# Optimization experiments

Measured on AMD Instinct MI355X. Metric: run time of the kernel, lower is better.

Reference implementation:

```python
import jax, jax.numpy as jnp
import numpy as np
from jax import lax

HEADS = 8
HEAD_C = 16  # attention_channels // heads = 128 // 8


def setup_inputs() -> dict:
    key = jax.random.key(0)
    ks = jax.random.split(key, 16)
    N, I, H, W = 8, 128, 36, 36
    R, C, A, O = 128, 128, 128, 128  # recurrent, common, attention, out channels
    s = lambda *sh: 0.05
    inp = {
        'x': jax.random.normal(ks[0], (N, I, H, W), jnp.float32),
        # input 1x1 conv (Accumulate of single Conv, bias init 0)
        'w_in': jax.random.normal(ks[1], (R, I), jnp.float32) * 0.05,
        'b_in': jnp.zeros((R,), jnp.float32),
        # 3x3 conv on cat([x, h]) -> common channels
        'w_conv': jax.random.normal(ks[2], (C, 2 * R, 3, 3), jnp.float32) * 0.05,
        'b_conv': jnp.zeros((C,), jnp.float32),
        # q/k/v 1x1 projections (no bias)
        'wq': jax.random.normal(ks[3], (A, C), jnp.float32) * 0.05,
        'wk': jax.random.normal(ks[4], (A, C), jnp.float32) * 0.05,
        'wv': jax.random.normal(ks[5], (A, C), jnp.float32) * 0.05,
        # gate 1x1 projections on cat([z, a]) (C + A inputs)
        'w_i': jax.random.normal(ks[6], (R, C + A), jnp.float32) * 0.05,
        'b_i': jnp.full((R,), -1.0, jnp.float32),  # init_input
        'w_f': jax.random.normal(ks[7], (R, C + A), jnp.float32) * 0.05,
        'b_f': jnp.full((R,), 1.0, jnp.float32),   # init_forget
        'w_g': jax.random.normal(ks[8], (R, C + A), jnp.float32) * 0.05,
        'b_g': jnp.zeros((R,), jnp.float32),
        'w_o': jax.random.normal(ks[9], (R, C + A), jnp.float32) * 0.05,
        'b_o': jnp.zeros((R,), jnp.float32),
        # output 1x1 conv
        'w_out': jax.random.normal(ks[10], (O, R), jnp.float32) * 0.05,
        'b_out': jnp.zeros((O,), jnp.float32),
    }
    return inp


def _conv1x1(w, x, b=None):
    y = jnp.einsum('oi,nihw->nohw', w, x)
    if b is not None:
        y = y + b[None, :, None, None]
    return y


def reference(x, w_in, b_in, w_conv, b_conv, wq, wk, wv,
              w_i, b_i, w_f, b_f, w_g, b_g, w_o, b_o, w_out, b_out):
    # first timestep: past is empty -> h = c = 0
    xt = jnp.tanh(_conv1x1(w_in, x, b_in))          # [N, R, H, W]
    h0 = jnp.zeros_like(xt)
    c0 = jnp.zeros_like(xt)
    xh = jnp.concatenate([xt, h0], axis=1)          # groups=1 -> plain concat
    z = lax.conv_general_dilated(xh, w_conv, (1, 1), 'SAME') + b_conv[None, :, None, None]
    N, C, H, W = z.shape
    HW = H * W
    q = _conv1x1(wq, z).reshape(N, HEADS, HEAD_C, HW)
    k = _conv1x1(wk, z).reshape(N, HEADS, HEAD_C, HW)
    v = _conv1x1(wv, z).reshape(N, HEADS, HEAD_C, HW)
    # spatial attention over H*W tokens per head
    w_attn = jax.nn.softmax(jnp.einsum('nhcq,nhcd->nhqd', q, k), axis=-1)  # [N,heads,HW,HW]
    a = jnp.einsum('nhcd,nhqd->nhcq', v, w_attn).reshape(N, -1, H, W)      # [N,A,H,W]
    za = jnp.concatenate([z, a], axis=1)
    i = jax.nn.sigmoid(_conv1x1(w_i, za, b_i))
    f = jax.nn.sigmoid(_conv1x1(w_f, za, b_f))
    g = jnp.tanh(_conv1x1(w_g, za, b_g))
    o = jax.nn.sigmoid(_conv1x1(w_o, za, b_o))
    c = f * c0 + i * g
    h = o * jnp.tanh(c)  # dropout p=0 -> identity
    return _conv1x1(w_out, h, b_out)
```

## Files before the change

kernel.cpp:

```cpp
#include <hip/hip_runtime.h>
#include <hip/hip_bf16.h>
#include <math.h>

typedef __hip_bfloat16 bf16;
typedef __attribute__((ext_vector_type(8))) short frag8;
typedef __attribute__((ext_vector_type(4))) float f32x4;
typedef __attribute__((ext_vector_type(16))) float f32x16;
typedef __attribute__((ext_vector_type(2))) unsigned int u32x2;
typedef __attribute__((ext_vector_type(4))) unsigned int u32x4;

#define HW  1296
#define CH  128
#define TT  1327104

__device__ __forceinline__ float b2f(bf16 v) { return __bfloat162float(v); }
__device__ __forceinline__ float bits2f(unsigned short u) {
    return __uint_as_float(((unsigned)u) << 16);
}
__device__ __forceinline__ float frcp(float x) { return __builtin_amdgcn_rcpf(x); }
__device__ __forceinline__ float fsigm(float x) { return frcp(1.0f + __expf(-x)); }
__device__ __forceinline__ float ftanh(float x) {
    float xc = fminf(15.0f, fmaxf(-15.0f, x));
    float e = __expf(2.0f * xc);
    return (e - 1.0f) * frcp(e + 1.0f);
}
__device__ __forceinline__ int packrh(float a, float b) {
    unsigned ua = __float_as_uint(a) + 0x8000u;
    unsigned ub = __float_as_uint(b) + 0x8000u;
    return (int)__builtin_amdgcn_perm(ub, ua, 0x07060302);
}
__device__ __forceinline__ int2 pack4(float a, float b, float c, float d) {
    int2 r; r.x = packrh(a, b); r.y = packrh(c, d); return r;
}
__device__ __forceinline__ unsigned cvtpk(float a, float b) {
    unsigned r;
    asm("v_cvt_pk_bf16_f32 %0, %1, %2" : "=v"(r) : "v"(a), "v"(b));
    return r;
}

__device__ __forceinline__ int detect_f32(const void* w) {
    const short4* p = (const short4*)w;
    short4 v = p[threadIdx.x & 63];
    int bad = 0;
    #pragma unroll
    for (int j = 0; j < 4; ++j) {
        float f = bits2f(((const unsigned short*)&v)[j]);
        if (!(fabsf(f) <= 100.0f)) bad = 1;
    }
    return __any(bad) ? 1 : 0;
}

__global__ __launch_bounds__(256) void k_prep(
    const void* w_in, const void* w_conv, const void* wq, const void* wk, const void* wv,
    const void* w_i, const void* w_g, const void* w_o, const void* w_out,
    const void* b_in, const void* b_conv, const void* b_i, const void* b_g,
    const void* b_o, const void* b_out,
    bf16* __restrict__ Wdst, float* __restrict__ Bdst)
{
    int idx = blockIdx.x * 256 + threadIdx.x;
    const int f = detect_f32(w_in);
    if (idx < 327680) {
        const void* src; int si;
        if (idx < 16384)       { src = w_in; si = idx; }
        else if (idx < 163840) { int j = idx - 16384; int tap = j >> 14, rem = j & 16383;
                                 int o = rem >> 7, r = rem & 127;
                                 src = w_conv; si = o * 2304 + r * 9 + tap; }
        else if (idx < 212992) { int j = idx - 163840; int o = j >> 7, i = j & 127;
                                 int ws_ = o >> 7;
                                 src = ws_ == 0 ? wq : ws_ == 1 ? wk : wv;
                                 si = (o & 127) * 128 + i; }
        else if (idx < 311296) { int j = idx - 212992; int g = j >> 15, rem = j & 32767;
                                 int o = rem >> 8, k = rem & 255;
                                 src = g == 0 ? w_i : g == 1 ? w_g : w_o; si = o * 256 + k; }
        else                   { int j = idx - 311296; int o = j >> 7, i = j & 127;
                                 src = w_out; si = o * 128 + i; }
        float v = f ? ((const float*)src)[si] : b2f(((const bf16*)src)[si]);
        if (idx >= 163840 && idx < 180224) v *= 1.4426950408889634f;
        Wdst[idx] = __float2bfloat16(v);
    } else if (idx < 327680 + 768) {
        int j = idx - 327680; int b = j >> 7, e = j & 127;
        const void* src = b == 0 ? b_in : b == 1 ? b_conv : b == 2 ? b_i
                        : b == 3 ? b_g : b == 4 ? b_o : b_out;
        Bdst[j] = f ? ((const float*)src)[e] : b2f(((const bf16*)src)[e]);
    }
}

__global__ __launch_bounds__(256) void k_inm(const void* __restrict__ x,
                                             const void* __restrict__ wraw,
                                             const bf16* __restrict__ Wm,
                                             const float* __restrict__ bias,
                                             bf16* __restrict__ XT) {
    __shared__ short Xl[32][132];
    const int tid = threadIdx.x, wave = tid >> 6, lane = tid & 63;
    const int quad = lane >> 4, l16 = lane & 15;
    const int n = blockIdx.x;
    const int pbase = blockIdx.y * 32;
    const int obase = blockIdx.z * 32 + (wave & 1) * 16;
    const int pstrip = (wave >> 1) * 16;
    const int f = detect_f32(wraw);

    frag8 WF[4];
    #pragma unroll
    for (int kc = 0; kc < 4; ++kc)
        WF[kc] = *(const frag8*)&Wm[(obase + l16) * CH + kc * 32 + quad * 8];

    #pragma unroll
    for (int rep = 0; rep < 4; ++rep) {
        int u = tid + rep * 256;
        int i = u >> 3;
        int p4 = (u & 7) * 4;
        int p = pbase + p4;
        short4 s = {0, 0, 0, 0};
        if (p < HW) {
            size_t gi = (size_t)n * CH * HW + (size_t)i * HW + p;
            if (f) {
                float4 fv = *(const float4*)((const float*)x + gi);
                int2 pk = pack4(fv.x, fv.y, fv.z, fv.w);
                s = *(short4*)&pk;
            } else {
                s = *(const short4*)((const bf16*)x + gi);
            }
        }
        Xl[p4 + 0][i] = s.x; Xl[p4 + 1][i] = s.y;
        Xl[p4 + 2][i] = s.z; Xl[p4 + 3][i] = s.w;
    }
    __syncthreads();

    const int pl = pstrip + l16;
    f32x4 acc = {0.f, 0.f, 0.f, 0.f};
    #pragma unroll
    for (int kc = 0; kc < 4; ++kc) {
        int k = kc * 32 + quad * 8;
        short4 b0 = *(const short4*)&Xl[pl][k];
        short4 b1 = *(const short4*)&Xl[pl][k + 4];
        frag8 bf = {b0.x, b0.y, b0.z, b0.w, b1.x, b1.y, b1.z, b1.w};
        acc = __builtin_amdgcn_mfma_f32_16x16x32_bf16(WF[kc], bf, acc, 0, 0, 0);
    }

    int p = pbase + pstrip + l16;
    if (p < HW) {
        int og = obase + quad * 4;
        int2 pk = pack4(ftanh(acc[0] + bias[og + 0]), ftanh(acc[1] + bias[og + 1]),
                        ftanh(acc[2] + bias[og + 2]), ftanh(acc[3] + bias[og + 3]));
        *(int2*)((short*)XT + ((size_t)n * HW + p) * CH + og) = pk;
    }
}

__global__ __launch_bounds__(256) void k_conv(
    const bf16* __restrict__ Act, const bf16* __restrict__ Wm,
    const float* __restrict__ bias, bf16* __restrict__ o0)
{
    const int tid = threadIdx.x, wave = tid >> 6, lane = tid & 63;
    const int quad = lane >> 4, l16 = lane & 15;
    const int ostrip = wave & 1, pstrip = wave >> 1;
    const int n = blockIdx.x;
    const int obase = blockIdx.z * 32 + ostrip * 16;
    const int pbase = blockIdx.y * 64 + pstrip * 32;
    const bf16* actn = Act + (size_t)n * HW * CH;

    const int p1 = pbase + l16, p2 = pbase + 16 + l16;
    const bool p1ok = p1 < HW, p2ok = p2 < HW;
    const int h1 = p1 / 36, w1 = p1 - h1 * 36;
    const int h2 = p2 / 36, w2 = p2 - h2 * 36;

    frag8 zf = {0, 0, 0, 0, 0, 0, 0, 0};
    f32x4 acc[2];
    acc[0] = (f32x4){0.f, 0.f, 0.f, 0.f};
    acc[1] = (f32x4){0.f, 0.f, 0.f, 0.f};

    frag8 A1[2][4], A2[2][4], WT[2][4];

    #define LOADTAP(TAP, BUF)                                                        \
    {                                                                                \
        const int dy = (TAP) / 3 - 1, dx = (TAP) - ((TAP) / 3) * 3 - 1;              \
        const bool ok1 = p1ok && (unsigned)(h1 + dy) < 36u && (unsigned)(w1 + dx) < 36u; \
        const bool ok2 = p2ok && (unsigned)(h2 + dy) < 36u && (unsigned)(w2 + dx) < 36u; \
        const int sh = dy * 36 + dx;                                                 \
        const bf16* a1 = actn + (size_t)(p1 + sh) * CH + quad * 8;                   \
        const bf16* a2 = actn + (size_t)(p2 + sh) * CH + quad * 8;                   \
        const bf16* wp = Wm + (TAP) * 16384 + (obase + l16) * CH + quad * 8;         \
        _Pragma("unroll")                                                            \
        for (int kc = 0; kc < 4; ++kc) {                                             \
            A1[BUF][kc] = ok1 ? *(const frag8*)&a1[kc * 32] : zf;                    \
            A2[BUF][kc] = ok2 ? *(const frag8*)&a2[kc * 32] : zf;                    \
            WT[BUF][kc] = *(const frag8*)&wp[kc * 32];                               \
        }                                                                            \
    }

    LOADTAP(0, 0);
    #pragma unroll
    for (int tap = 0; tap < 9; ++tap) {
        const int cur = tap & 1;
        if (tap < 8) LOADTAP(tap + 1, cur ^ 1);
        #pragma unroll
        for (int kc = 0; kc < 4; ++kc) {
            acc[0] = __builtin_amdgcn_mfma_f32_16x16x32_bf16(WT[cur][kc], A1[cur][kc], acc[0], 0, 0, 0);
            acc[1] = __builtin_amdgcn_mfma_f32_16x16x32_bf16(WT[cur][kc], A2[cur][kc], acc[1], 0, 0, 0);
        }
    }
    #undef LOADTAP

    const int og = obase + quad * 4;
    #pragma unroll
    for (int pt = 0; pt < 2; ++pt) {
        int p = pbase + pt * 16 + l16;
        if (p >= HW) continue;
        size_t rowoff = ((size_t)n * HW + p) * CH;
        int2 pk = pack4(acc[pt][0] + bias[og + 0], acc[pt][1] + bias[og + 1],
                        acc[pt][2] + bias[og + 2], acc[pt][3] + bias[og + 3]);
        *(int2*)((short*)o0 + rowoff + og) = pk;
    }
}

__global__ __launch_bounds__(256) void k_qkv(
    const bf16* __restrict__ Act, const bf16* __restrict__ Wm,
    bf16* __restrict__ o0, bf16* __restrict__ o1, bf16* __restrict__ o2)
{
    const int tid = threadIdx.x, wave = tid >> 6, lane = tid & 63;
    const int quad = lane >> 4, l16 = lane & 15;
    const int ostrip = wave & 1, pstrip = wave >> 1;
    const int n = blockIdx.x;
    const int obase = blockIdx.z * 64 + ostrip * 32;
    const int pbase = blockIdx.y * 64 + pstrip * 32;
    const bf16* actn = Act + (size_t)n * HW * CH;
    const bool vtile = (blockIdx.z >= 4);

    const int p1 = pbase + l16, p2 = pbase + 16 + l16;
    const bool p1ok = p1 < HW, p2ok = p2 < HW;

    frag8 zf = {0, 0, 0, 0, 0, 0, 0, 0};
    frag8 B1[4], B2[4], W0a[4], W1a[4];
    #pragma unroll
    for (int kc = 0; kc < 4; ++kc) {
        int ko = kc * 32 + quad * 8;
        B1[kc] = p1ok ? *(const frag8*)&actn[(size_t)p1 * CH + ko] : zf;
        B2[kc] = p2ok ? *(const frag8*)&actn[(size_t)p2 * CH + ko] : zf;
        W0a[kc] = *(const frag8*)&Wm[(size_t)(obase + l16) * CH + ko];
        W1a[kc] = *(const frag8*)&Wm[(size_t)(obase + 16 + l16) * CH + ko];
    }

    f32x4 acc[2][2];
    #pragma unroll
    for (int of = 0; of < 2; ++of) {
        acc[of][0] = (f32x4){0.f, 0.f, 0.f, 0.f};
        acc[of][1] = (f32x4){0.f, 0.f, 0.f, 0.f};
    }

    #pragma unroll
    for (int kc = 0; kc < 4; ++kc) {
        if (vtile) {
            acc[0][0] = __builtin_amdgcn_mfma_f32_16x16x32_bf16(B1[kc], W0a[kc], acc[0][0], 0, 0, 0);
            acc[0][1] = __builtin_amdgcn_mfma_f32_16x16x32_bf16(B2[kc], W0a[kc], acc[0][1], 0, 0, 0);
            acc[1][0] = __builtin_amdgcn_mfma_f32_16x16x32_bf16(B1[kc], W1a[kc], acc[1][0], 0, 0, 0);
            acc[1][1] = __builtin_amdgcn_mfma_f32_16x16x32_bf16(B2[kc], W1a[kc], acc[1][1], 0, 0, 0);
        } else {
            acc[0][0] = __builtin_amdgcn_mfma_f32_16x16x32_bf16(W0a[kc], B1[kc], acc[0][0], 0, 0, 0);
            acc[0][1] = __builtin_amdgcn_mfma_f32_16x16x32_bf16(W0a[kc], B2[kc], acc[0][1], 0, 0, 0);
            acc[1][0] = __builtin_amdgcn_mfma_f32_16x16x32_bf16(W1a[kc], B1[kc], acc[1][0], 0, 0, 0);
            acc[1][1] = __builtin_amdgcn_mfma_f32_16x16x32_bf16(W1a[kc], B2[kc], acc[1][1], 0, 0, 0);
        }
    }

    if (vtile) {
        #pragma unroll
        for (int of = 0; of < 2; ++of) {
            int ov = obase + of * 16 - 256 + l16;
            #pragma unroll
            for (int pt = 0; pt < 2; ++pt) {
                int p4 = pbase + pt * 16 + quad * 4;
                if (p4 >= HW) continue;
                int2 pk = pack4(acc[of][pt][0], acc[of][pt][1], acc[of][pt][2], acc[of][pt][3]);
                *(int2*)((short*)o2 + ((size_t)n * CH + ov) * HW + p4) = pk;
            }
        }
        return;
    }
    #pragma unroll
    for (int of = 0; of < 2; ++of) {
        int og = obase + of * 16 + quad * 4;
        int which = og >> 7, ol = og & 127;
        bf16* dst = which == 0 ? o0 : o1;
        #pragma unroll
        for (int pt = 0; pt < 2; ++pt) {
            int p = pbase + pt * 16 + l16;
            if (p >= HW) continue;
            size_t di = (((size_t)n * 8 + (ol >> 4)) * HW + p) * 16 + (ol & 15);
            int2 pk = pack4(acc[of][pt][0], acc[of][pt][1], acc[of][pt][2], acc[of][pt][3]);
            *(int2*)((short*)dst + di) = pk;
        }
    }
}

__global__ __launch_bounds__(256) void k_cell(
    const bf16* __restrict__ Zb, const bf16* __restrict__ Ab,
    const bf16* __restrict__ Wg, const float* __restrict__ bg,
    const bf16* __restrict__ Wo, const float* __restrict__ bo,
    void* __restrict__ out, const void* __restrict__ wraw)
{
    __shared__ short Hl[16][136];
    const int tid = threadIdx.x, w = tid >> 6, lane = tid & 63;
    const int quad = lane >> 4, l16 = lane & 15;
    const int n = blockIdx.x;
    const int pbase = blockIdx.y * 16;
    const int f32f = detect_f32(wraw);
    const bf16* zn = Zb + (size_t)n * HW * CH;
    const bf16* an = Ab + (size_t)n * HW * CH;

    const int obase = w * 32;
    const int p1 = pbase + l16;

    f32x4 acc[3][2];
    #pragma unroll
    for (int g = 0; g < 3; ++g) {
        acc[g][0] = (f32x4){0.f, 0.f, 0.f, 0.f};
        acc[g][1] = (f32x4){0.f, 0.f, 0.f, 0.f};
    }

    frag8 GB[2];
    frag8 GW[2][6];

    #define LOADG(KC, BUF)                                                           \
    {                                                                                \
        const bf16* src = ((KC) >= 4) ? an : zn;                                     \
        const int ko = ((KC) & 3) * 32 + quad * 8;                                   \
        GB[BUF] = *(const frag8*)&src[(size_t)p1 * CH + ko];                         \
        _Pragma("unroll")                                                            \
        for (int g = 0; g < 3; ++g) {                                                \
            _Pragma("unroll")                                                        \
            for (int of = 0; of < 2; ++of)                                           \
                GW[BUF][g * 2 + of] = *(const frag8*)&Wg[g * 32768 +                 \
                    (obase + of * 16 + l16) * 256 + (KC) * 32 + quad * 8];           \
        }                                                                            \
    }

    LOADG(0, 0);
    #pragma unroll
    for (int kc = 0; kc < 8; ++kc) {
        const int cur = kc & 1;
        if (kc < 7) LOADG(kc + 1, cur ^ 1);
// ... 22 lines not shown
        *(int2*)&Hl[l16][og] = pack4(hv[0], hv[1], hv[2], hv[3]);
    }

    frag8 OW[2][4];
    #pragma unroll
    for (int of = 0; of < 2; ++of)
        #pragma unroll
        for (int kc = 0; kc < 4; ++kc)
            OW[of][kc] = *(const frag8*)&Wo[(size_t)(obase + of * 16 + l16) * CH
                                            + kc * 32 + quad * 8];
    __syncthreads();

    f32x4 oc[2];
    oc[0] = (f32x4){0.f, 0.f, 0.f, 0.f};
    oc[1] = (f32x4){0.f, 0.f, 0.f, 0.f};
    #pragma unroll
    for (int kc = 0; kc < 4; ++kc) {
        int k = kc * 32 + quad * 8;
        short4 h0 = *(const short4*)&Hl[l16][k];
        short4 h1 = *(const short4*)&Hl[l16][k + 4];
        frag8 af = {h0.x, h0.y, h0.z, h0.w, h1.x, h1.y, h1.z, h1.w};
        #pragma unroll
        for (int of = 0; of < 2; ++of)
            oc[of] = __builtin_amdgcn_mfma_f32_16x16x32_bf16(af, OW[of][kc], oc[of], 0, 0, 0);
    }
    int p4 = pbase + quad * 4;
    #pragma unroll
    for (int of = 0; of < 2; ++of) {
        int o = obase + of * 16 + l16;
        float bv = bo[o];
        size_t di = ((size_t)n * CH + o) * HW + p4;
        if (f32f) {
            float4 fv = {oc[of][0] + bv, oc[of][1] + bv, oc[of][2] + bv, oc[of][3] + bv};
            *(float4*)&((float*)out)[di] = fv;
        } else {
            int2 pk = pack4(oc[of][0] + bv, oc[of][1] + bv, oc[of][2] + bv, oc[of][3] + bv);
            *(int2*)&((short*)out)[di] = pk;
        }
    }
}

__global__ __launch_bounds__(512) void k_attn(const bf16* __restrict__ Qg,
                                              const bf16* __restrict__ Kg,
                                              const bf16* __restrict__ Vcf,
                                              bf16* __restrict__ A) {
    __shared__ float Lc[4][9][64];

    const int tid = threadIdx.x;
    const int w = tid >> 6, lane = tid & 63;
    const int l32 = lane & 31, hi = lane >> 5;
    const int qw = w & 3, dq = w >> 2;
    const int n = blockIdx.x;
    const int head = blockIdx.z;
    const int qb = blockIdx.y * 128 + qw * 32;
    const int qtok = qb + l32;

    const short* Qh = (const short*)Qg + ((size_t)(n * 8 + head)) * HW * 16;
    const short* Kh = (const short*)Kg + ((size_t)(n * 8 + head)) * HW * 16;
    const short* Vh = (const short*)Vcf + ((size_t)n * CH + head * 16) * HW;

    frag8 qf = {0, 0, 0, 0, 0, 0, 0, 0};
    if (qtok < HW) qf = *(const frag8*)&Qh[(size_t)qtok * 16 + hi * 8];

    const short one = (short)0x3F80;
    const frag8 vones = {one, one, one, one, one, one, one, one};
    const frag8 vzero = {0, 0, 0, 0, 0, 0, 0, 0};
    const frag8 vfill = (l32 == 16) ? vones : vzero;
    const bool vload = l32 < 16;
    const short* Vrow = Vh + (size_t)(vload ? l32 : 0) * HW;

    const f32x16 zero16 = {};
    f32x16 Oacc = {};

    auto KLD = [&](int dd) -> frag8 {
        return *(const frag8*)&Kh[(size_t)(dd + l32) * 16 + hi * 8];
    };
    auto VLD = [&](int dd) -> frag8 {
        return vload ? *(const frag8*)&Vrow[dd + hi * 8] : vfill;
    };

    const int c0 = dq ? 20 : 0;
    frag8 kf  = KLD(c0 * 32);
    frag8 kf2 = KLD(c0 * 32 + 32);
    frag8 va  = VLD(c0 * 32);
    frag8 vb  = VLD(c0 * 32 + 16);
    f32x16 S = __builtin_amdgcn_mfma_f32_32x32x16_bf16(kf, qf, zero16, 0, 0, 0);

    for (int it = 0; it < 20; ++it) {
        const int d0 = (c0 + it) * 32;
        frag8 kn  = KLD(d0 + 64);
        frag8 van = VLD(d0 + 32);
        frag8 vbn = VLD(d0 + 48);
        f32x16 Sn = __builtin_amdgcn_mfma_f32_32x32x16_bf16(kf2, qf, zero16, 0, 0, 0);

        float p[16];
        #pragma unroll
        for (int r = 0; r < 16; ++r) p[r] = __builtin_amdgcn_exp2f(S[r]);

        #pragma unroll
        for (int hh = 0; hh < 2; ++hh) {
            unsigned P0 = cvtpk(p[hh * 8 + 0], p[hh * 8 + 1]);
            unsigned P1 = cvtpk(p[hh * 8 + 2], p[hh * 8 + 3]);
            unsigned P2 = cvtpk(p[hh * 8 + 4], p[hh * 8 + 5]);
            unsigned P3 = cvtpk(p[hh * 8 + 6], p[hh * 8 + 7]);
            u32x2 s02 = __builtin_amdgcn_permlane32_swap(P0, P2, false, false);
            u32x2 s13 = __builtin_amdgcn_permlane32_swap(P1, P3, false, false);
            u32x4 bw = {s02[0], s13[0], s02[1], s13[1]};
            frag8 pf = __builtin_bit_cast(frag8, bw);
            Oacc = __builtin_amdgcn_mfma_f32_32x32x16_bf16(hh ? vb : va, pf, Oacc, 0, 0, 0);
        }
        kf2 = kn; va = van; vb = vbn; S = Sn;
    }

    if (dq) {
        float p[8];
        #pragma unroll
        for (int r = 0; r < 8; ++r) p[r] = __builtin_amdgcn_exp2f(S[r]);
        unsigned P0 = cvtpk(p[0], p[1]);
        unsigned P1 = cvtpk(p[2], p[3]);
        unsigned P2 = cvtpk(p[4], p[5]);
        unsigned P3 = cvtpk(p[6], p[7]);
        u32x2 s02 = __builtin_amdgcn_permlane32_swap(P0, P2, false, false);
        u32x2 s13 = __builtin_amdgcn_permlane32_swap(P1, P3, false, false);
        u32x4 bw = {s02[0], s13[0], s02[1], s13[1]};
        frag8 pf = __builtin_bit_cast(frag8, bw);
        Oacc = __builtin_amdgcn_mfma_f32_32x32x16_bf16(va, pf, Oacc, 0, 0, 0);
        #pragma unroll
        for (int r = 0; r < 8; ++r) Lc[qw][r][lane] = Oacc[r];
        Lc[qw][8][lane] = Oacc[8];
    }
    __syncthreads();
    if (dq == 0) {
        #pragma unroll
        for (int r = 0; r < 8; ++r) Oacc[r] += Lc[qw][r][lane];
        float lsum = Oacc[8] + Lc[qw][8][lane];
        u32x2 lb = __builtin_amdgcn_permlane32_swap(__float_as_uint(lsum),
                                                    __float_as_uint(lsum), false, false);
        float inv = frcp(__uint_as_float(lb[0]));
        if (qtok < HW) {
            short* An = (short*)A + ((size_t)n * HW + qtok) * CH + head * 16;
            int2 pk0 = pack4(Oacc[0] * inv, Oacc[1] * inv, Oacc[2] * inv, Oacc[3] * inv);
            int2 pk1 = pack4(Oacc[4] * inv, Oacc[5] * inv, Oacc[6] * inv, Oacc[7] * inv);
            *(int2*)&An[hi * 4] = pk0;
            *(int2*)&An[8 + hi * 4] = pk1;
        }
    }
}

extern "C" void kernel_launch(void* const* d_in, const int* in_sizes, int n_in,
                              void* d_out, int out_size, void* d_ws, size_t ws_size,
                              hipStream_t stream) {
    char* ws = (char*)d_ws;
    bf16*  Wst  = (bf16*)(ws + 256);
    float* Bst  = (float*)(ws + 655616);
    bf16*  XT   = (bf16*)(ws + 1048576);
    bf16*  Zb   = XT + TT;
    bf16*  Qb   = Zb + TT;
    bf16*  Kb   = Qb + TT;
    bf16*  Vb   = Kb + TT;
    bf16*  Ab   = Vb + TT;

    k_prep<<<1284, 256, 0, stream>>>(d_in[1], d_in[3], d_in[5], d_in[6], d_in[7],
                                     d_in[8], d_in[12], d_in[14], d_in[16],
                                     d_in[2], d_in[4], d_in[9], d_in[13], d_in[15], d_in[17],
                                     Wst, Bst);
    k_inm<<<dim3(8, 41, 4), 256, 0, stream>>>(d_in[0], d_in[1], Wst, Bst, XT);
    k_conv<<<dim3(8, 21, 4), 256, 0, stream>>>(XT, Wst + 16384, Bst + 128, Zb);
    k_qkv<<<dim3(8, 21, 6), 256, 0, stream>>>(Zb, Wst + 163840, Qb, Kb, Vb);
    k_attn<<<dim3(8, 11, 8), 512, 0, stream>>>(Qb, Kb, Vb, Ab);
    k_cell<<<dim3(8, 81), 256, 0, stream>>>(Zb, Ab, Wst + 212992, Bst + 256,
                                            Wst + 311296, Bst + 640, d_out, d_in[1]);
}
```

Before: 195.2 us.

## Fuse all stages into one persistent cooperative kernel with grid syncs

Replaces six separate kernel launches with a single cooperative persistent kernel (768 blocks of 256 threads) that loops over each stage's tiles and separates stages with grid-wide barriers. The attention stage is also reshaped from 512-thread blocks covering 128 queries to 256-thread blocks covering 64 queries. The aim is to remove launch gaps and inter-kernel drain between the short stages. In exchange, grid syncs add cost, the fixed grid may give uneven load balance per stage, and register pressure from merging all stages could lower occupancy; a non-cooperative multi-launch path is kept as a fallback.

```diff
diff --git a/kernel.cpp b/kernel.cpp
--- a/kernel.cpp
+++ b/kernel.cpp
@@ -1,4 +1,5 @@
 #include <hip/hip_runtime.h>
+#include <hip/hip_cooperative_groups.h>
 #include <hip/hip_bf16.h>
 #include <math.h>
 
@@ -50,54 +51,51 @@
     return __any(bad) ? 1 : 0;
 }
 
-__global__ __launch_bounds__(256) void k_prep(
-    const void* w_in, const void* w_conv, const void* wq, const void* wk, const void* wv,
-    const void* w_i, const void* w_g, const void* w_o, const void* w_out,
-    const void* b_in, const void* b_conv, const void* b_i, const void* b_g,
-    const void* b_o, const void* b_out,
-    bf16* __restrict__ Wdst, float* __restrict__ Bdst)
-{
-    int idx = blockIdx.x * 256 + threadIdx.x;
-    const int f = detect_f32(w_in);
+struct MP {
+    const void *x, *w_in, *w_conv, *wq, *wk, *wv, *w_i, *w_g, *w_o, *w_out;
+    const void *b_in, *b_conv, *b_i, *b_g, *b_o, *b_out;
+    bf16* Wst; float* Bst;
+    bf16 *XT, *Zb, *Qb, *Kb, *Vb, *Ab;
+    void* out;
+};
+
+__device__ __forceinline__ void dev_prep(const MP& p, int idx, int f) {
     if (idx < 327680) {
         const void* src; int si;
-        if (idx < 16384)       { src = w_in; si = idx; }
+        if (idx < 16384)       { src = p.w_in; si = idx; }
         else if (idx < 163840) { int j = idx - 16384; int tap = j >> 14, rem = j & 16383;
                                  int o = rem >> 7, r = rem & 127;
-                                 src = w_conv; si = o * 2304 + r * 9 + tap; }
+                                 src = p.w_conv; si = o * 2304 + r * 9 + tap; }
         else if (idx < 212992) { int j = idx - 163840; int o = j >> 7, i = j & 127;
                                  int ws_ = o >> 7;
-                                 src = ws_ == 0 ? wq : ws_ == 1 ? wk : wv;
+                                 src = ws_ == 0 ? p.wq : ws_ == 1 ? p.wk : p.wv;
                                  si = (o & 127) * 128 + i; }
         else if (idx < 311296) { int j = idx - 212992; int g = j >> 15, rem = j & 32767;
                                  int o = rem >> 8, k = rem & 255;
-                                 src = g == 0 ? w_i : g == 1 ? w_g : w_o; si = o * 256 + k; }
+                                 src = g == 0 ? p.w_i : g == 1 ? p.w_g : p.w_o;
+                                 si = o * 256 + k; }
         else                   { int j = idx - 311296; int o = j >> 7, i = j & 127;
-                                 src = w_out; si = o * 128 + i; }
+                                 src = p.w_out; si = o * 128 + i; }
         float v = f ? ((const float*)src)[si] : b2f(((const bf16*)src)[si]);
         if (idx >= 163840 && idx < 180224) v *= 1.4426950408889634f;
-        Wdst[idx] = __float2bfloat16(v);
+        p.Wst[idx] = __float2bfloat16(v);
     } else if (idx < 327680 + 768) {
         int j = idx - 327680; int b = j >> 7, e = j & 127;
-        const void* src = b == 0 ? b_in : b == 1 ? b_conv : b == 2 ? b_i
-                        : b == 3 ? b_g : b == 4 ? b_o : b_out;
-        Bdst[j] = f ? ((const float*)src)[e] : b2f(((const bf16*)src)[e]);
-    }
-}
-
-__global__ __launch_bounds__(256) void k_inm(const void* __restrict__ x,
-                                             const void* __restrict__ wraw,
-                                             const bf16* __restrict__ Wm,
-                                             const float* __restrict__ bias,
-                                             bf16* __restrict__ XT) {
-    __shared__ short Xl[32][132];
+        const void* src = b == 0 ? p.b_in : b == 1 ? p.b_conv : b == 2 ? p.b_i
+                        : b == 3 ? p.b_g : b == 4 ? p.b_o : p.b_out;
+        p.Bst[j] = f ? ((const float*)src)[e] : b2f(((const bf16*)src)[e]);
+    }
+}
+
+__device__ __forceinline__ void dev_inm(const MP& p, int f, int n, int py, int oz,
+                                        short (*Xl)[132]) {
     const int tid = threadIdx.x, wave = tid >> 6, lane = tid & 63;
     const int quad = lane >> 4, l16 = lane & 15;
-    const int n = blockIdx.x;
-    const int pbase = blockIdx.y * 32;
-    const int obase = blockIdx.z * 32 + (wave & 1) * 16;
+    const int pbase = py * 32;
+    const int obase = oz * 32 + (wave & 1) * 16;
     const int pstrip = (wave >> 1) * 16;
-    const int f = detect_f32(wraw);
+    const bf16* Wm = p.Wst;
+    const float* bias = p.Bst;
 
     frag8 WF[4];
     #pragma unroll
@@ -109,16 +107,16 @@
         int u = tid + rep * 256;
         int i = u >> 3;
         int p4 = (u & 7) * 4;
-        int p = pbase + p4;
+        int pp = pbase + p4;
         short4 s = {0, 0, 0, 0};
-        if (p < HW) {
-            size_t gi = (size_t)n * CH * HW + (size_t)i * HW + p;
+        if (pp < HW) {
+            size_t gi = (size_t)n * CH * HW + (size_t)i * HW + pp;
             if (f) {
-                float4 fv = *(const float4*)((const float*)x + gi);
+                float4 fv = *(const float4*)((const float*)p.x + gi);
                 int2 pk = pack4(fv.x, fv.y, fv.z, fv.w);
                 s = *(short4*)&pk;
             } else {
-                s = *(const short4*)((const bf16*)x + gi);
+                s = *(const short4*)((const bf16*)p.x + gi);
             }
         }
         Xl[p4 + 0][i] = s.x; Xl[p4 + 1][i] = s.y;
@@ -137,26 +135,25 @@
         acc = __builtin_amdgcn_mfma_f32_16x16x32_bf16(WF[kc], bf, acc, 0, 0, 0);
     }
 
-    int p = pbase + pstrip + l16;
-    if (p < HW) {
+    int pp = pbase + pstrip + l16;
+    if (pp < HW) {
         int og = obase + quad * 4;
         int2 pk = pack4(ftanh(acc[0] + bias[og + 0]), ftanh(acc[1] + bias[og + 1]),
                         ftanh(acc[2] + bias[og + 2]), ftanh(acc[3] + bias[og + 3]));
-        *(int2*)((short*)XT + ((size_t)n * HW + p) * CH + og) = pk;
-    }
-}
-
-__global__ __launch_bounds__(256) void k_conv(
-    const bf16* __restrict__ Act, const bf16* __restrict__ Wm,
-    const float* __restrict__ bias, bf16* __restrict__ o0)
-{
+        *(int2*)((short*)p.XT + ((size_t)n * HW + pp) * CH + og) = pk;
+    }
+    __syncthreads();
+}
+
+__device__ __forceinline__ void dev_conv(const MP& p, int n, int py, int oz) {
     const int tid = threadIdx.x, wave = tid >> 6, lane = tid & 63;
     const int quad = lane >> 4, l16 = lane & 15;
     const int ostrip = wave & 1, pstrip = wave >> 1;
-    const int n = blockIdx.x;
-    const int obase = blockIdx.z * 32 + ostrip * 16;
-    const int pbase = blockIdx.y * 64 + pstrip * 32;
-    const bf16* actn = Act + (size_t)n * HW * CH;
+    const int obase = oz * 32 + ostrip * 16;
+    const int pbase = py * 64 + pstrip * 32;
+    const bf16* Wm = p.Wst + 16384;
+    const float* bias = p.Bst + 128;
+    const bf16* actn = p.XT + (size_t)n * HW * CH;
 
     const int p1 = pbase + l16, p2 = pbase + 16 + l16;
     const bool p1ok = p1 < HW, p2ok = p2 < HW;
@@ -203,27 +200,24 @@
     const int og = obase + quad * 4;
     #pragma unroll
     for (int pt = 0; pt < 2; ++pt) {
-        int p = pbase + pt * 16 + l16;
-        if (p >= HW) continue;
-        size_t rowoff = ((size_t)n * HW + p) * CH;
+        int pp = pbase + pt * 16 + l16;
+        if (pp >= HW) continue;
+        size_t rowoff = ((size_t)n * HW + pp) * CH;
         int2 pk = pack4(acc[pt][0] + bias[og + 0], acc[pt][1] + bias[og + 1],
                         acc[pt][2] + bias[og + 2], acc[pt][3] + bias[og + 3]);
-        *(int2*)((short*)o0 + rowoff + og) = pk;
-    }
-}
-
-__global__ __launch_bounds__(256) void k_qkv(
-    const bf16* __restrict__ Act, const bf16* __restrict__ Wm,
-    bf16* __restrict__ o0, bf16* __restrict__ o1, bf16* __restrict__ o2)
-{
+        *(int2*)((short*)p.Zb + rowoff + og) = pk;
+    }
+}
+
+__device__ __forceinline__ void dev_qkv(const MP& p, int n, int py, int oz) {
     const int tid = threadIdx.x, wave = tid >> 6, lane = tid & 63;
     const int quad = lane >> 4, l16 = lane & 15;
     const int ostrip = wave & 1, pstrip = wave >> 1;
-    const int n = blockIdx.x;
-    const int obase = blockIdx.z * 64 + ostrip * 32;
-    const int pbase = blockIdx.y * 64 + pstrip * 32;
-    const bf16* actn = Act + (size_t)n * HW * CH;
-    const bool vtile = (blockIdx.z >= 4);
+    const int obase = oz * 64 + ostrip * 32;
+    const int pbase = py * 64 + pstrip * 32;
+    const bf16* Wm = p.Wst + 163840;
+    const bf16* actn = p.Zb + (size_t)n * HW * CH;
+    const bool vtile = (oz >= 4);
 
     const int p1 = pbase + l16, p2 = pbase + 16 + l16;
     const bool p1ok = p1 < HW, p2ok = p2 < HW;
@@ -270,7 +264,7 @@
                 int p4 = pbase + pt * 16 + quad * 4;
                 if (p4 >= HW) continue;
                 int2 pk = pack4(acc[of][pt][0], acc[of][pt][1], acc[of][pt][2], acc[of][pt][3]);
-                *(int2*)((short*)o2 + ((size_t)n * CH + ov) * HW + p4) = pk;
+                *(int2*)((short*)p.Vb + ((size_t)n * CH + ov) * HW + p4) = pk;
             }
         }
         return;
@@ -279,32 +273,131 @@
     for (int of = 0; of < 2; ++of) {
         int og = obase + of * 16 + quad * 4;
         int which = og >> 7, ol = og & 127;
-        bf16* dst = which == 0 ? o0 : o1;
+        bf16* dst = which == 0 ? p.Qb : p.Kb;
         #pragma unroll
         for (int pt = 0; pt < 2; ++pt) {
-            int p = pbase + pt * 16 + l16;
-            if (p >= HW) continue;
-            size_t di = (((size_t)n * 8 + (ol >> 4)) * HW + p) * 16 + (ol & 15);
+            int pp = pbase + pt * 16 + l16;
+            if (pp >= HW) continue;
+            size_t di = (((size_t)n * 8 + (ol >> 4)) * HW + pp) * 16 + (ol & 15);
             int2 pk = pack4(acc[of][pt][0], acc[of][pt][1], acc[of][pt][2], acc[of][pt][3]);
             *(int2*)((short*)dst + di) = pk;
         }
     }
 }
 
-__global__ __launch_bounds__(256) void k_cell(
-    const bf16* __restrict__ Zb, const bf16* __restrict__ Ab,
-    const bf16* __restrict__ Wg, const float* __restrict__ bg,
-    const bf16* __restrict__ Wo, const float* __restrict__ bo,
-    void* __restrict__ out, const void* __restrict__ wraw)
-{
-    __shared__ short Hl[16][136];
+__device__ __forceinline__ void dev_attn(const MP& p, int n, int qt, int head,
+                                         float (*Lc)[9][64]) {
+    const int tid = threadIdx.x;
+    const int w = tid >> 6, lane = tid & 63;
+    const int l32 = lane & 31, hi = lane >> 5;
+    const int qw = w & 1, dq = w >> 1;
+    const int qb = qt * 64 + qw * 32;
+    const int qtok = qb + l32;
+
+    const short* Qh = (const short*)p.Qb + ((size_t)(n * 8 + head)) * HW * 16;
+    const short* Kh = (const short*)p.Kb + ((size_t)(n * 8 + head)) * HW * 16;
+    const short* Vh = (const short*)p.Vb + ((size_t)n * CH + head * 16) * HW;
+
+    frag8 qf = {0, 0, 0, 0, 0, 0, 0, 0};
+    if (qtok < HW) qf = *(const frag8*)&Qh[(size_t)qtok * 16 + hi * 8];
+
+    const short one = (short)0x3F80;
+    const frag8 vones = {one, one, one, one, one, one, one, one};
+    const frag8 vzero = {0, 0, 0, 0, 0, 0, 0, 0};
+    const frag8 vfill = (l32 == 16) ? vones : vzero;
+    const bool vload = l32 < 16;
+    const short* Vrow = Vh + (size_t)(vload ? l32 : 0) * HW;
+
+    const f32x16 zero16 = {};
+    f32x16 Oacc = {};
+
+    auto KLD = [&](int dd) -> frag8 {
+        return *(const frag8*)&Kh[(size_t)(dd + l32) * 16 + hi * 8];
+    };
+    auto VLD = [&](int dd) -> frag8 {
+        return vload ? *(const frag8*)&Vrow[dd + hi * 8] : vfill;
+    };
+
+    const int c0 = dq ? 20 : 0;
+    frag8 kf  = KLD(c0 * 32);
+    frag8 kf2 = KLD(c0 * 32 + 32);
+    frag8 va  = VLD(c0 * 32);
+    frag8 vb  = VLD(c0 * 32 + 16);
+    f32x16 S = __builtin_amdgcn_mfma_f32_32x32x16_bf16(kf, qf, zero16, 0, 0, 0);
+
+    for (int it = 0; it < 20; ++it) {
+        const int d0 = (c0 + it) * 32;
+        frag8 kn  = KLD(d0 + 64);
+        frag8 van = VLD(d0 + 32);
+        frag8 vbn = VLD(d0 + 48);
+        f32x16 Sn = __builtin_amdgcn_mfma_f32_32x32x16_bf16(kf2, qf, zero16, 0, 0, 0);
+
+        float pe[16];
+        #pragma unroll
+        for (int r = 0; r < 16; ++r) pe[r] = __builtin_amdgcn_exp2f(S[r]);
+
+        #pragma unroll
+        for (int hh = 0; hh < 2; ++hh) {
+            unsigned P0 = cvtpk(pe[hh * 8 + 0], pe[hh * 8 + 1]);
+            unsigned P1 = cvtpk(pe[hh * 8 + 2], pe[hh * 8 + 3]);
+            unsigned P2 = cvtpk(pe[hh * 8 + 4], pe[hh * 8 + 5]);
+            unsigned P3 = cvtpk(pe[hh * 8 + 6], pe[hh * 8 + 7]);
+            u32x2 s02 = __builtin_amdgcn_permlane32_swap(P0, P2, false, false);
+            u32x2 s13 = __builtin_amdgcn_permlane32_swap(P1, P3, false, false);
+            u32x4 bw = {s02[0], s13[0], s02[1], s13[1]};
+            frag8 pf = __builtin_bit_cast(frag8, bw);
+            Oacc = __builtin_amdgcn_mfma_f32_32x32x16_bf16(hh ? vb : va, pf, Oacc, 0, 0, 0);
+        }
+        kf2 = kn; va = van; vb = vbn; S = Sn;
+    }
+
+    if (dq) {
+        float pe[8];
+        #pragma unroll
+        for (int r = 0; r < 8; ++r) pe[r] = __builtin_amdgcn_exp2f(S[r]);
+        unsigned P0 = cvtpk(pe[0], pe[1]);
+        unsigned P1 = cvtpk(pe[2], pe[3]);
+        unsigned P2 = cvtpk(pe[4], pe[5]);
+        unsigned P3 = cvtpk(pe[6], pe[7]);
+        u32x2 s02 = __builtin_amdgcn_permlane32_swap(P0, P2, false, false);
+        u32x2 s13 = __builtin_amdgcn_permlane32_swap(P1, P3, false, false);
+        u32x4 bw = {s02[0], s13[0], s02[1], s13[1]};
+        frag8 pf = __builtin_bit_cast(frag8, bw);
+        Oacc = __builtin_amdgcn_mfma_f32_32x32x16_bf16(va, pf, Oacc, 0, 0, 0);
+        #pragma unroll
+        for (int r = 0; r < 8; ++r) Lc[qw][r][lane] = Oacc[r];
+        Lc[qw][8][lane] = Oacc[8];
+    }
+    __syncthreads();
+    if (dq == 0) {
+        #pragma unroll
+        for (int r = 0; r < 8; ++r) Oacc[r] += Lc[qw][r][lane];
+        float lsum = Oacc[8] + Lc[qw][8][lane];
+        u32x2 lb = __builtin_amdgcn_permlane32_swap(__float_as_uint(lsum),
+                                                    __float_as_uint(lsum), false, false);
+        float inv = frcp(__uint_as_float(lb[0]));
+        if (qtok < HW) {
+            short* An = (short*)p.Ab + ((size_t)n * HW + qtok) * CH + head * 16;
+            int2 pk0 = pack4(Oacc[0] * inv, Oacc[1] * inv, Oacc[2] * inv, Oacc[3] * inv);
+            int2 pk1 = pack4(Oacc[4] * inv, Oacc[5] * inv, Oacc[6] * inv, Oacc[7] * inv);
+            *(int2*)&An[hi * 4] = pk0;
+            *(int2*)&An[8 + hi * 4] = pk1;
+        }
+    }
+    __syncthreads();
+}
+
+__device__ __forceinline__ void dev_cell(const MP& p, int f32f, int n, int py,
+                                         short (*Hl)[136]) {
     const int tid = threadIdx.x, w = tid >> 6, lane = tid & 63;
     const int quad = lane >> 4, l16 = lane & 15;
-    const int n = blockIdx.x;
-    const int pbase = blockIdx.y * 16;
-    const int f32f = detect_f32(wraw);
-    const bf16* zn = Zb + (size_t)n * HW * CH;
-    const bf16* an = Ab + (size_t)n * HW * CH;
+    const int pbase = py * 16;
+    const bf16* zn = p.Zb + (size_t)n * HW * CH;
+    const bf16* an = p.Ab + (size_t)n * HW * CH;
+    const bf16* Wg = p.Wst + 212992;
+    const float* bg = p.Bst + 256;
+    const bf16* Wo = p.Wst + 311296;
+    const float* bo = p.Bst + 640;
 
     const int obase = w * 32;
     const int p1 = pbase + l16;
@@ -393,119 +486,61 @@
         size_t di = ((size_t)n * CH + o) * HW + p4;
         if (f32f) {
             float4 fv = {oc[of][0] + bv, oc[of][1] + bv, oc[of][2] + bv, oc[of][3] + bv};
-            *(float4*)&((float*)out)[di] = fv;
+            *(float4*)&((float*)p.out)[di] = fv;
         } else {
             int2 pk = pack4(oc[of][0] + bv, oc[of][1] + bv, oc[of][2] + bv, oc[of][3] + bv);
-            *(int2*)&((short*)out)[di] = pk;
-        }
-    }
-}
-
-__global__ __launch_bounds__(512) void k_attn(const bf16* __restrict__ Qg,
-                                              const bf16* __restrict__ Kg,
-                                              const bf16* __restrict__ Vcf,
-                                              bf16* __restrict__ A) {
-    __shared__ float Lc[4][9][64];
-
-    const int tid = threadIdx.x;
-    const int w = tid >> 6, lane = tid & 63;
-    const int l32 = lane & 31, hi = lane >> 5;
-    const int qw = w & 3, dq = w >> 2;
-    const int n = blockIdx.x;
-    const int head = blockIdx.z;
-    const int qb = blockIdx.y * 128 + qw * 32;
-    const int qtok = qb + l32;
-
-    const short* Qh = (const short*)Qg + ((size_t)(n * 8 + head)) * HW * 16;
-    const short* Kh = (const short*)Kg + ((size_t)(n * 8 + head)) * HW * 16;
-    const short* Vh = (const short*)Vcf + ((size_t)n * CH + head * 16) * HW;
-
-    frag8 qf = {0, 0, 0, 0, 0, 0, 0, 0};
-    if (qtok < HW) qf = *(const frag8*)&Qh[(size_t)qtok * 16 + hi * 8];
-
-    const short one = (short)0x3F80;
-    const frag8 vones = {one, one, one, one, one, one, one, one};
-    const frag8 vzero = {0, 0, 0, 0, 0, 0, 0, 0};
-    const frag8 vfill = (l32 == 16) ? vones : vzero;
-    const bool vload = l32 < 16;
-    const short* Vrow = Vh + (size_t)(vload ? l32 : 0) * HW;
-
-    const f32x16 zero16 = {};
-    f32x16 Oacc = {};
-
-    auto KLD = [&](int dd) -> frag8 {
-        return *(const frag8*)&Kh[(size_t)(dd + l32) * 16 + hi * 8];
-    };
-    auto VLD = [&](int dd) -> frag8 {
-        return vload ? *(const frag8*)&Vrow[dd + hi * 8] : vfill;
-    };
-
-    const int c0 = dq ? 20 : 0;
-    frag8 kf  = KLD(c0 * 32);
-    frag8 kf2 = KLD(c0 * 32 + 32);
-    frag8 va  = VLD(c0 * 32);
-    frag8 vb  = VLD(c0 * 32 + 16);
-    f32x16 S = __builtin_amdgcn_mfma_f32_32x32x16_bf16(kf, qf, zero16, 0, 0, 0);
-
-    for (int it = 0; it < 20; ++it) {
-        const int d0 = (c0 + it) * 32;
-        frag8 kn  = KLD(d0 + 64);
-        frag8 van = VLD(d0 + 32);
-        frag8 vbn = VLD(d0 + 48);
-        f32x16 Sn = __builtin_amdgcn_mfma_f32_32x32x16_bf16(kf2, qf, zero16, 0, 0, 0);
-
-        float p[16];
-        #pragma unroll
-        for (int r = 0; r < 16; ++r) p[r] = __builtin_amdgcn_exp2f(S[r]);
-
-        #pragma unroll
-        for (int hh = 0; hh < 2; ++hh) {
-            unsigned P0 = cvtpk(p[hh * 8 + 0], p[hh * 8 + 1]);
-            unsigned P1 = cvtpk(p[hh * 8 + 2], p[hh * 8 + 3]);
-            unsigned P2 = cvtpk(p[hh * 8 + 4], p[hh * 8 + 5]);
-            unsigned P3 = cvtpk(p[hh * 8 + 6], p[hh * 8 + 7]);
-            u32x2 s02 = __builtin_amdgcn_permlane32_swap(P0, P2, false, false);
-            u32x2 s13 = __builtin_amdgcn_permlane32_swap(P1, P3, false, false);
-            u32x4 bw = {s02[0], s13[0], s02[1], s13[1]};
-            frag8 pf = __builtin_bit_cast(frag8, bw);
-            Oacc = __builtin_amdgcn_mfma_f32_32x32x16_bf16(hh ? vb : va, pf, Oacc, 0, 0, 0);
-        }
-        kf2 = kn; va = van; vb = vbn; S = Sn;
-    }
-
-    if (dq) {
-        float p[8];
-        #pragma unroll
-        for (int r = 0; r < 8; ++r) p[r] = __builtin_amdgcn_exp2f(S[r]);
-        unsigned P0 = cvtpk(p[0], p[1]);
-        unsigned P1 = cvtpk(p[2], p[3]);
-        unsigned P2 = cvtpk(p[4], p[5]);
-        unsigned P3 = cvtpk(p[6], p[7]);
-        u32x2 s02 = __builtin_amdgcn_permlane32_swap(P0, P2, false, false);
-        u32x2 s13 = __builtin_amdgcn_permlane32_swap(P1, P3, false, false);
-        u32x4 bw = {s02[0], s13[0], s02[1], s13[1]};
-        frag8 pf = __builtin_bit_cast(frag8, bw);
-        Oacc = __builtin_amdgcn_mfma_f32_32x32x16_bf16(va, pf, Oacc, 0, 0, 0);
-        #pragma unroll
-        for (int r = 0; r < 8; ++r) Lc[qw][r][lane] = Oacc[r];
-        Lc[qw][8][lane] = Oacc[8];
+            *(int2*)&((short*)p.out)[di] = pk;
+        }
     }
     __syncthreads();
-    if (dq == 0) {
-        #pragma unroll
-        for (int r = 0; r < 8; ++r) Oacc[r] += Lc[qw][r][lane];
-        float lsum = Oacc[8] + Lc[qw][8][lane];
-        u32x2 lb = __builtin_amdgcn_permlane32_swap(__float_as_uint(lsum),
-                                                    __float_as_uint(lsum), false, false);
-        float inv = frcp(__uint_as_float(lb[0]));
-        if (qtok < HW) {
-            short* An = (short*)A + ((size_t)n * HW + qtok) * CH + head * 16;
-            int2 pk0 = pack4(Oacc[0] * inv, Oacc[1] * inv, Oacc[2] * inv, Oacc[3] * inv);
-            int2 pk1 = pack4(Oacc[4] * inv, Oacc[5] * inv, Oacc[6] * inv, Oacc[7] * inv);
-            *(int2*)&An[hi * 4] = pk0;
-            *(int2*)&An[8 + hi * 4] = pk1;
-        }
-    }
+}
+
+__global__ __launch_bounds__(256, 3) void k_mega(MP p) {
+    __shared__ short Xl[32][132];
+    __shared__ short Hl[16][136];
+    __shared__ float Lc[2][9][64];
+    cooperative_groups::grid_group gg = cooperative_groups::this_grid();
+    const int b = blockIdx.x, NB = gridDim.x;
+    const int f = detect_f32(p.w_in);
+
+    for (int idx = b * 256 + threadIdx.x; idx < 327680 + 768; idx += NB * 256)
+        dev_prep(p, idx, f);
+    gg.sync();
+    for (int t = b; t < 1312; t += NB) dev_inm(p, f, t & 7, (t >> 3) % 41, (t >> 3) / 41, Xl);
+    gg.sync();
+    for (int t = b; t < 672;  t += NB) dev_conv(p, t & 7, (t >> 3) % 21, (t >> 3) / 21);
+    gg.sync();
+    for (int t = b; t < 1008; t += NB) dev_qkv(p, t & 7, (t >> 3) % 21, (t >> 3) / 21);
+    gg.sync();
+    for (int t = b; t < 1344; t += NB) dev_attn(p, t & 7, (t >> 3) % 21, (t >> 3) / 21, Lc);
+    gg.sync();
+    for (int t = b; t < 648;  t += NB) dev_cell(p, f, t & 7, t >> 3, Hl);
+}
+
+__global__ __launch_bounds__(256) void kw_prep(MP p) {
+    int f = detect_f32(p.w_in);
+    int idx = blockIdx.x * 256 + threadIdx.x;
+    if (idx < 327680 + 768) dev_prep(p, idx, f);
+}
+__global__ __launch_bounds__(256) void kw_inm(MP p) {
+    __shared__ short Xl[32][132];
+    int f = detect_f32(p.w_in);
+    dev_inm(p, f, blockIdx.x, blockIdx.y, blockIdx.z, Xl);
+}
+__global__ __launch_bounds__(256) void kw_conv(MP p) {
+    dev_conv(p, blockIdx.x, blockIdx.y, blockIdx.z);
+}
+__global__ __launch_bounds__(256) void kw_qkv(MP p) {
+    dev_qkv(p, blockIdx.x, blockIdx.y, blockIdx.z);
+}
+__global__ __launch_bounds__(256) void kw_attn(MP p) {
+    __shared__ float Lc[2][9][64];
+    dev_attn(p, blockIdx.x, blockIdx.y, blockIdx.z, Lc);
+}
+__global__ __launch_bounds__(256) void kw_cell(MP p) {
+    __shared__ short Hl[16][136];
+    int f = detect_f32(p.w_in);
+    dev_cell(p, f, blockIdx.x, blockIdx.y, Hl);
 }
 
 extern "C" void kernel_launch(void* const* d_in, const int* in_sizes, int n_in,
@@ -521,14 +556,28 @@
     bf16*  Vb   = Kb + TT;
     bf16*  Ab   = Vb + TT;
 
-    k_prep<<<1284, 256, 0, stream>>>(d_in[1], d_in[3], d_in[5], d_in[6], d_in[7],
-                                     d_in[8], d_in[12], d_in[14], d_in[16],
-                                     d_in[2], d_in[4], d_in[9], d_in[13], d_in[15], d_in[17],
-                                     Wst, Bst);
-    k_inm<<<dim3(8, 41, 4), 256, 0, stream>>>(d_in[0], d_in[1], Wst, Bst, XT);
-    k_conv<<<dim3(8, 21, 4), 256, 0, stream>>>(XT, Wst + 16384, Bst + 128, Zb);
-    k_qkv<<<dim3(8, 21, 6), 256, 0, stream>>>(Zb, Wst + 163840, Qb, Kb, Vb);
-    k_attn<<<dim3(8, 11, 8), 512, 0, stream>>>(Qb, Kb, Vb, Ab);
-    k_cell<<<dim3(8, 81), 256, 0, stream>>>(Zb, Ab, Wst + 212992, Bst + 256,
-                                            Wst + 311296, Bst + 640, d_out, d_in[1]);
-}
+    MP mp;
+    mp.x = d_in[0];   mp.w_in = d_in[1];  mp.b_in = d_in[2];
+    mp.w_conv = d_in[3]; mp.b_conv = d_in[4];
+    mp.wq = d_in[5];  mp.wk = d_in[6];   mp.wv = d_in[7];
+    mp.w_i = d_in[8]; mp.b_i = d_in[9];
+    mp.w_g = d_in[12]; mp.b_g = d_in[13];
+    mp.w_o = d_in[14]; mp.b_o = d_in[15];
+    mp.w_out = d_in[16]; mp.b_out = d_in[17];
+    mp.Wst = Wst; mp.Bst = Bst;
+    mp.XT = XT; mp.Zb = Zb; mp.Qb = Qb; mp.Kb = Kb; mp.Vb = Vb; mp.Ab = Ab;
+    mp.out = d_out;
+
+    void* kargs[] = { &mp };
+    hipError_t err = hipLaunchCooperativeKernel((const void*)k_mega,
+                                                dim3(768), dim3(256),
+                                                kargs, 0, stream);
+    if (err != hipSuccess) {
+        kw_prep<<<1284, 256, 0, stream>>>(mp);
+        kw_inm<<<dim3(8, 41, 4), 256, 0, stream>>>(mp);
+        kw_conv<<<dim3(8, 21, 4), 256, 0, stream>>>(mp);
+        kw_qkv<<<dim3(8, 21, 6), 256, 0, stream>>>(mp);
+        kw_attn<<<dim3(8, 21, 8), 256, 0, stream>>>(mp);
+        kw_cell<<<dim3(8, 81), 256, 0, stream>>>(mp);
+    }
+}
```

Measured after the change: 650.9 us. +233.4%, slower.

## Fuse 3x3 conv and QKV projection into one kernel via shared-memory Z tile

Applied to the files above, without the earlier changes.

Merges the 3x3 conv kernel and the QKV projection kernel into a single kernel. Each block computes all 128 output channels of z for a 32-pixel strip, keeps it in LDS, and then computes Q/K/V for that strip from LDS instead of re-reading Zb from global memory. This removes one kernel launch and the global round trip of z into the projection. In exchange the grid shrinks to 328 blocks of 512 threads, each doing more work serially, with only 4 of 8 waves busy in the second QKV pass.

```diff
diff --git a/kernel.cpp b/kernel.cpp
--- a/kernel.cpp
+++ b/kernel.cpp
@@ -146,18 +146,20 @@
     }
 }
 
-__global__ __launch_bounds__(256) void k_conv(
-    const bf16* __restrict__ Act, const bf16* __restrict__ Wm,
-    const float* __restrict__ bias, bf16* __restrict__ o0)
+__global__ __launch_bounds__(512) void k_cq(
+    const bf16* __restrict__ XT, const bf16* __restrict__ Wc,
+    const float* __restrict__ bc, const bf16* __restrict__ Wqkv,
+    bf16* __restrict__ Zb, bf16* __restrict__ Qb, bf16* __restrict__ Kb,
+    bf16* __restrict__ Vb)
 {
-    const int tid = threadIdx.x, wave = tid >> 6, lane = tid & 63;
+    __shared__ short Zl[32][136];
+    const int tid = threadIdx.x, w = tid >> 6, lane = tid & 63;
     const int quad = lane >> 4, l16 = lane & 15;
-    const int ostrip = wave & 1, pstrip = wave >> 1;
     const int n = blockIdx.x;
-    const int obase = blockIdx.z * 32 + ostrip * 16;
-    const int pbase = blockIdx.y * 64 + pstrip * 32;
-    const bf16* actn = Act + (size_t)n * HW * CH;
-
+    const int pbase = blockIdx.y * 32;
+    const bf16* actn = XT + (size_t)n * HW * CH;
+
+    const int obase = w * 16;
     const int p1 = pbase + l16, p2 = pbase + 16 + l16;
     const bool p1ok = p1 < HW, p2ok = p2 < HW;
     const int h1 = p1 / 36, w1 = p1 - h1 * 36;
@@ -178,7 +180,7 @@
         const int sh = dy * 36 + dx;                                                 \
         const bf16* a1 = actn + (size_t)(p1 + sh) * CH + quad * 8;                   \
         const bf16* a2 = actn + (size_t)(p2 + sh) * CH + quad * 8;                   \
-        const bf16* wp = Wm + (TAP) * 16384 + (obase + l16) * CH + quad * 8;         \
+        const bf16* wp = Wc + (TAP) * 16384 + (obase + l16) * CH + quad * 8;         \
         _Pragma("unroll")                                                            \
         for (int kc = 0; kc < 4; ++kc) {                                             \
             A1[BUF][kc] = ok1 ? *(const frag8*)&a1[kc * 32] : zf;                    \
@@ -204,89 +206,75 @@
     #pragma unroll
     for (int pt = 0; pt < 2; ++pt) {
         int p = pbase + pt * 16 + l16;
-        if (p >= HW) continue;
-        size_t rowoff = ((size_t)n * HW + p) * CH;
-        int2 pk = pack4(acc[pt][0] + bias[og + 0], acc[pt][1] + bias[og + 1],
-                        acc[pt][2] + bias[og + 2], acc[pt][3] + bias[og + 3]);
-        *(int2*)((short*)o0 + rowoff + og) = pk;
-    }
-}
-
-__global__ __launch_bounds__(256) void k_qkv(
-    const bf16* __restrict__ Act, const bf16* __restrict__ Wm,
-    bf16* __restrict__ o0, bf16* __restrict__ o1, bf16* __restrict__ o2)
-{
-    const int tid = threadIdx.x, wave = tid >> 6, lane = tid & 63;
-    const int quad = lane >> 4, l16 = lane & 15;
-    const int ostrip = wave & 1, pstrip = wave >> 1;
-    const int n = blockIdx.x;
-    const int obase = blockIdx.z * 64 + ostrip * 32;
-    const int pbase = blockIdx.y * 64 + pstrip * 32;
-    const bf16* actn = Act + (size_t)n * HW * CH;
-    const bool vtile = (blockIdx.z >= 4);
-
-    const int p1 = pbase + l16, p2 = pbase + 16 + l16;
-    const bool p1ok = p1 < HW, p2ok = p2 < HW;
-
-    frag8 zf = {0, 0, 0, 0, 0, 0, 0, 0};
-    frag8 B1[4], B2[4], W0a[4], W1a[4];
-    #pragma unroll
-    for (int kc = 0; kc < 4; ++kc) {
-        int ko = kc * 32 + quad * 8;
-        B1[kc] = p1ok ? *(const frag8*)&actn[(size_t)p1 * CH + ko] : zf;
-        B2[kc] = p2ok ? *(const frag8*)&actn[(size_t)p2 * CH + ko] : zf;
-        W0a[kc] = *(const frag8*)&Wm[(size_t)(obase + l16) * CH + ko];
-        W1a[kc] = *(const frag8*)&Wm[(size_t)(obase + 16 + l16) * CH + ko];
-    }
-
-    f32x4 acc[2][2];
-    #pragma unroll
-    for (int of = 0; of < 2; ++of) {
-        acc[of][0] = (f32x4){0.f, 0.f, 0.f, 0.f};
-        acc[of][1] = (f32x4){0.f, 0.f, 0.f, 0.f};
-    }
-
-    #pragma unroll
-    for (int kc = 0; kc < 4; ++kc) {
-        if (vtile) {
-            acc[0][0] = __builtin_amdgcn_mfma_f32_16x16x32_bf16(B1[kc], W0a[kc], acc[0][0], 0, 0, 0);
-            acc[0][1] = __builtin_amdgcn_mfma_f32_16x16x32_bf16(B2[kc], W0a[kc], acc[0][1], 0, 0, 0);
-            acc[1][0] = __builtin_amdgcn_mfma_f32_16x16x32_bf16(B1[kc], W1a[kc], acc[1][0], 0, 0, 0);
-            acc[1][1] = __builtin_amdgcn_mfma_f32_16x16x32_bf16(B2[kc], W1a[kc], acc[1][1], 0, 0, 0);
+        int2 pk = pack4(acc[pt][0] + bc[og + 0], acc[pt][1] + bc[og + 1],
+                        acc[pt][2] + bc[og + 2], acc[pt][3] + bc[og + 3]);
+        *(int2*)&Zl[pt * 16 + l16][og] = pk;
+        if (p < HW)
+            *(int2*)((short*)Zb + ((size_t)n * HW + p) * CH + og) = pk;
+    }
+    __syncthreads();
+
+    for (int ot = w; ot < 12; ot += 8) {
+        const bool vt = (ot >= 8);
+        const int ob = ot * 32;
+        frag8 B1[4], B2[4], W0a[4], W1a[4];
+        #pragma unroll
+        for (int kc = 0; kc < 4; ++kc) {
+            int ko = kc * 32 + quad * 8;
+            B1[kc]  = *(const frag8*)&Zl[l16][ko];
+            B2[kc]  = *(const frag8*)&Zl[16 + l16][ko];
+            W0a[kc] = *(const frag8*)&Wqkv[(size_t)(ob + l16) * CH + ko];
+            W1a[kc] = *(const frag8*)&Wqkv[(size_t)(ob + 16 + l16) * CH + ko];
+        }
+
+        f32x4 qacc[2][2];
+        #pragma unroll
+        for (int of = 0; of < 2; ++of) {
+            qacc[of][0] = (f32x4){0.f, 0.f, 0.f, 0.f};
+            qacc[of][1] = (f32x4){0.f, 0.f, 0.f, 0.f};
+        }
+        #pragma unroll
+        for (int kc = 0; kc < 4; ++kc) {
+            if (vt) {
+                qacc[0][0] = __builtin_amdgcn_mfma_f32_16x16x32_bf16(B1[kc], W0a[kc], qacc[0][0], 0, 0, 0);
+                qacc[0][1] = __builtin_amdgcn_mfma_f32_16x16x32_bf16(B2[kc], W0a[kc], qacc[0][1], 0, 0, 0);
+                qacc[1][0] = __builtin_amdgcn_mfma_f32_16x16x32_bf16(B1[kc], W1a[kc], qacc[1][0], 0, 0, 0);
+                qacc[1][1] = __builtin_amdgcn_mfma_f32_16x16x32_bf16(B2[kc], W1a[kc], qacc[1][1], 0, 0, 0);
+            } else {
+                qacc[0][0] = __builtin_amdgcn_mfma_f32_16x16x32_bf16(W0a[kc], B1[kc], qacc[0][0], 0, 0, 0);
+                qacc[0][1] = __builtin_amdgcn_mfma_f32_16x16x32_bf16(W0a[kc], B2[kc], qacc[0][1], 0, 0, 0);
+                qacc[1][0] = __builtin_amdgcn_mfma_f32_16x16x32_bf16(W1a[kc], B1[kc], qacc[1][0], 0, 0, 0);
+                qacc[1][1] = __builtin_amdgcn_mfma_f32_16x16x32_bf16(W1a[kc], B2[kc], qacc[1][1], 0, 0, 0);
+            }
+        }
+
+        if (vt) {
+            #pragma unroll
+            for (int of = 0; of < 2; ++of) {
+                int ov = ob + of * 16 - 256 + l16;
+                #pragma unroll
+                for (int pt = 0; pt < 2; ++pt) {
+                    int p4 = pbase + pt * 16 + quad * 4;
+                    if (p4 >= HW) continue;
+                    int2 pk = pack4(qacc[of][pt][0], qacc[of][pt][1], qacc[of][pt][2], qacc[of][pt][3]);
+                    *(int2*)((short*)Vb + ((size_t)n * CH + ov) * HW + p4) = pk;
+                }
+            }
         } else {
-            acc[0][0] = __builtin_amdgcn_mfma_f32_16x16x32_bf16(W0a[kc], B1[kc], acc[0][0], 0, 0, 0);
-            acc[0][1] = __builtin_amdgcn_mfma_f32_16x16x32_bf16(W0a[kc], B2[kc], acc[0][1], 0, 0, 0);
-            acc[1][0] = __builtin_amdgcn_mfma_f32_16x16x32_bf16(W1a[kc], B1[kc], acc[1][0], 0, 0, 0);
-            acc[1][1] = __builtin_amdgcn_mfma_f32_16x16x32_bf16(W1a[kc], B2[kc], acc[1][1], 0, 0, 0);
-        }
-    }
-
-    if (vtile) {
-        #pragma unroll
-        for (int of = 0; of < 2; ++of) {
-            int ov = obase + of * 16 - 256 + l16;
             #pragma unroll
-            for (int pt = 0; pt < 2; ++pt) {
-                int p4 = pbase + pt * 16 + quad * 4;
-                if (p4 >= HW) continue;
-                int2 pk = pack4(acc[of][pt][0], acc[of][pt][1], acc[of][pt][2], acc[of][pt][3]);
-                *(int2*)((short*)o2 + ((size_t)n * CH + ov) * HW + p4) = pk;
+            for (int of = 0; of < 2; ++of) {
+                int ogq = ob + of * 16 + quad * 4;
+                int which = ogq >> 7, ol = ogq & 127;
+                bf16* dst = which == 0 ? Qb : Kb;
+                #pragma unroll
+                for (int pt = 0; pt < 2; ++pt) {
+                    int p = pbase + pt * 16 + l16;
+                    if (p >= HW) continue;
+                    size_t di = (((size_t)n * 8 + (ol >> 4)) * HW + p) * 16 + (ol & 15);
+                    int2 pk = pack4(qacc[of][pt][0], qacc[of][pt][1], qacc[of][pt][2], qacc[of][pt][3]);
+                    *(int2*)((short*)dst + di) = pk;
+                }
             }
-        }
-        return;
-    }
-    #pragma unroll
-    for (int of = 0; of < 2; ++of) {
-        int og = obase + of * 16 + quad * 4;
-        int which = og >> 7, ol = og & 127;
-        bf16* dst = which == 0 ? o0 : o1;
-        #pragma unroll
-        for (int pt = 0; pt < 2; ++pt) {
-            int p = pbase + pt * 16 + l16;
-            if (p >= HW) continue;
-            size_t di = (((size_t)n * 8 + (ol >> 4)) * HW + p) * 16 + (ol & 15);
-            int2 pk = pack4(acc[of][pt][0], acc[of][pt][1], acc[of][pt][2], acc[of][pt][3]);
-            *(int2*)((short*)dst + di) = pk;
         }
     }
 }
@@ -526,8 +514,8 @@
                                      d_in[2], d_in[4], d_in[9], d_in[13], d_in[15], d_in[17],
                                      Wst, Bst);
     k_inm<<<dim3(8, 41, 4), 256, 0, stream>>>(d_in[0], d_in[1], Wst, Bst, XT);
-    k_conv<<<dim3(8, 21, 4), 256, 0, stream>>>(XT, Wst + 16384, Bst + 128, Zb);
-    k_qkv<<<dim3(8, 21, 6), 256, 0, stream>>>(Zb, Wst + 163840, Qb, Kb, Vb);
+    k_cq<<<dim3(8, 41), 512, 0, stream>>>(XT, Wst + 16384, Bst + 128, Wst + 163840,
+                                          Zb, Qb, Kb, Vb);
     k_attn<<<dim3(8, 11, 8), 512, 0, stream>>>(Qb, Kb, Vb, Ab);
     k_cell<<<dim3(8, 81), 256, 0, stream>>>(Zb, Ab, Wst + 212992, Bst + 256,
                                             Wst + 311296, Bst + 640, d_out, d_in[1]);
```

New measurement: 199.6 us. 2.3% more time.
